# Kernel optimization log

Measured on AMD Instinct MI355X. Metric: run time of the kernel, lower is better.

The kernel has to match this reference:

```python
import jax, jax.numpy as jnp
import numpy as np

B, NELEC, NAO, NMO, NCONF, L = 128, 192, 128, 96, 32, 80
SCALE = 0.12  # keeps det of LxL matrices in float32 range


def setup_inputs() -> dict:
    key = jax.random.key(0)
    k1, k2, k3 = jax.random.split(key, 3)
    ao = jax.random.normal(k1, (B, NELEC, NAO), jnp.float32) * SCALE
    mo_w = jax.random.normal(k2, (NMO, NAO), jnp.float32) * SCALE  # Linear(nao->nmo) weight
    ci_w = jax.random.normal(k3, (1, NCONF), jnp.float32)          # Linear(nconf->1) weight
    # Configs: each config singly-occupies L distinct spatial orbitals (occ==1 branch
    # of get_index_configs -> spin-orbital index 2*i). Even, distinct, sorted indices.
    rng = np.random.default_rng(0)
    spatial = np.stack([np.sort(rng.permutation(NMO)[:L]) for _ in range(NCONF)])
    conf_idx = jnp.asarray(2 * spatial, dtype=jnp.int32)  # [NCONF, L], values < NELEC
    return {"ao": ao, "mo_w": mo_w, "ci_w": ci_w, "conf_idx": conf_idx}


def reference(ao, mo_w, ci_w, conf_idx):
    # layer_mo: mo = ao @ W^T  -> [B, NELEC, NMO]
    mo = jnp.einsum('ben,mn->bem', ao, mo_w)
    # duplicate_orbitals: stack/view/t/view == repeat each spatial orbital twice along columns
    dup = jnp.repeat(mo, 2, axis=2)  # [B, NELEC, 2*NMO]
    # SlaterPooling: gather rows and cols by the same config index, then determinant
    sub = dup[:, conf_idx[:, :, None], conf_idx[:, None, :]]  # [B, NCONF, L, L]
    dets = jnp.linalg.det(sub)  # [B, NCONF]  (batched LU)
    # layer_ci: CI-coefficient contraction -> [B, 1]
    return dets @ ci_w.T
```

## Files before the change

kernel.cpp:

```cpp
#include <hip/hip_runtime.h>

#define B_    128
#define NELEC 192
#define NAO   128
#define NMO   96
#define NCONF 32
#define L_    80

__global__ void zero_out_k(float* out) { if (threadIdx.x < B_) out[threadIdx.x] = 0.f; }

__global__ __launch_bounds__(256) void gemm_g_k(const float* __restrict__ ao,
                                                const float* __restrict__ mo_w,
                                                float* __restrict__ G) {
    int b  = blockIdx.x;
    int st = blockIdx.y;
    int tid = threadIdx.x;
    int s_local = tid >> 4;
    int m0 = (tid & 15) * 6;
    int s = st * 16 + s_local;
    const float* arow = ao + ((size_t)b * NELEC + 2 * s) * NAO;
    const float* w0   = mo_w + (size_t)m0 * NAO;
    float acc[6] = {0.f, 0.f, 0.f, 0.f, 0.f, 0.f};
    for (int n = 0; n < NAO; n += 4) {
        float4 av = *(const float4*)(arow + n);
#pragma unroll
        for (int q = 0; q < 6; ++q) {
            float4 wv = *(const float4*)(w0 + (size_t)q * NAO + n);
            acc[q] += av.x * wv.x + av.y * wv.y + av.z * wv.z + av.w * wv.w;
        }
    }
    float* grow = G + ((size_t)b * NMO + s) * NMO + m0;
#pragma unroll
    for (int q = 0; q < 6; ++q) grow[q] = acc[q];
}

__device__ __forceinline__ float rdlane(float x, int src) {
    return __int_as_float(__builtin_amdgcn_readlane(__float_as_int(x), src));
}
__device__ __forceinline__ int rdlanei(int x, int src) {
    return __builtin_amdgcn_readlane(x, src);
}
#define DPPMAX(v, ctrl)                                                          \
    v = fmaxf(v, __int_as_float(__builtin_amdgcn_update_dpp(                     \
            __float_as_int(v), __float_as_int(v), (ctrl), 0xf, 0xf, false)))

template <bool USE_G>
__global__ __launch_bounds__(64) void det_reg_k(const float* __restrict__ ao,
                                                const float* __restrict__ mo_w,
                                                const float* __restrict__ G,
                                                const float* __restrict__ ci_w,
                                                const int* __restrict__ conf_idx,
                                                float* __restrict__ out) {
    __shared__ __align__(16) float Ms[40][84];
    __shared__ int sIdx[L_];
    __shared__ int tbl[64];

    int c = blockIdx.x;
    int b = blockIdx.y;
    int lane = threadIdx.x;

    if (lane < 64) sIdx[lane] = conf_idx[c * L_ + lane] >> 1;
    if (lane < 16) sIdx[64 + lane] = conf_idx[c * L_ + 64 + lane] >> 1;
    __syncthreads();

    float a[81];
#pragma unroll
    for (int t = 0; t < 81; ++t) a[t] = 0.f;

    const float* Gb = G + (size_t)b * NMO * NMO;

#pragma unroll 1
    for (int pass = 0; pass < 2; ++pass) {
        int r0 = pass * 40;
        for (int e = lane; e < 40 * L_; e += 64) {
            int i = e / L_, j = e - i * L_;
            float v;
            if (USE_G) {
                v = Gb[(size_t)sIdx[r0 + i] * NMO + sIdx[j]];
            } else {
                const float* ar = ao + ((size_t)b * NELEC + 2 * sIdx[r0 + i]) * NAO;
                const float* wr = mo_w + (size_t)sIdx[j] * NAO;
                float acc = 0.f;
                for (int n = 0; n < NAO; n += 4) {
                    float4 av = *(const float4*)(ar + n);
                    float4 wv = *(const float4*)(wr + n);
                    acc += av.x * wv.x + av.y * wv.y + av.z * wv.z + av.w * wv.w;
                }
                v = acc;
            }
            Ms[i][j] = v;
        }
        __syncthreads();
        if (pass == 0) {
            if (lane < 40) {
#pragma unroll
                for (int q = 0; q < 20; ++q) {
                    float4 v4 = *(const float4*)&Ms[lane][4 * q];
                    a[4 * q] = v4.x; a[4 * q + 1] = v4.y; a[4 * q + 2] = v4.z; a[4 * q + 3] = v4.w;
                }
            }
        } else {
            if (lane >= 40) {
#pragma unroll
                for (int q = 0; q < 20; ++q) {
                    float4 v4 = *(const float4*)&Ms[lane - 40][4 * q];
                    a[4 * q] = v4.x; a[4 * q + 1] = v4.y; a[4 * q + 2] = v4.z; a[4 * q + 3] = v4.w;
                }
            }
        }
        __syncthreads();
    }

    double det = 1.0;
    int inv = 0;
    bool act = true;

#pragma unroll 1
    for (int k = 0; k < 16; ++k) {
        int rem = 79 - k;
        float cand = act ? fabsf(a[0]) : -1.f;
        float m = cand;
        DPPMAX(m, 0x111); DPPMAX(m, 0x112); DPPMAX(m, 0x114); DPPMAX(m, 0x118);
        DPPMAX(m, 0x142); DPPMAX(m, 0x143);
        float mx = rdlane(m, 63);
        unsigned long long sel = __ballot(act && cand == mx);
        int p = __ffsll(sel) - 1;

        inv += __popcll(__ballot(act && lane < p));

        float piv = rdlane(a[0], p);
        det *= (double)piv;
        if (lane == p) act = false;
        float la = (act && piv != 0.f) ? a[0] / piv : 0.f;

        if (lane < 16) {
            float* Brow = &Ms[24 + lane][0];
            float4 Qc = *(const float4*)&Brow[0];
            float lb = (piv != 0.f) ? Qc.x / piv : 0.f;
#pragma unroll
            for (int tb = 0; tb < 5; ++tb) {
                if (16 * tb < rem) {
#pragma unroll
                    for (int j = 0; j < 4; ++j) {
                        float4 Qn = *(const float4*)&Brow[16 * tb + 4 * j + 4];
                        float4 W;
                        W.x = fmaf(-lb, rdlane(a[16 * tb + 4 * j + 1], p), Qc.y);
                        W.y = fmaf(-lb, rdlane(a[16 * tb + 4 * j + 2], p), Qc.z);
                        W.z = fmaf(-lb, rdlane(a[16 * tb + 4 * j + 3], p), Qc.w);
                        W.w = fmaf(-lb, rdlane(a[16 * tb + 4 * j + 4], p), Qn.x);
                        *(float4*)&Brow[16 * tb + 4 * j] = W;
                        Qc = Qn;
                    }
                }
            }
        }

#pragma unroll
        for (int tb = 0; tb < 5; ++tb) {
            if (16 * tb < rem) {
#pragma unroll
                for (int i = 0; i < 16; ++i) {
                    float u = rdlane(a[16 * tb + i + 1], p);
                    a[16 * tb + i] = fmaf(-la, u, a[16 * tb + i + 1]);
                }
            }
        }
    }

    unsigned long long mask_a = __ballot(act);
    int rank = __popcll(mask_a & ((1ull << lane) - 1));
    if (act) tbl[rank] = lane;
    __syncthreads();
    int srcl = tbl[lane & 63];
    int src2 = (lane < 48) ? srcl : lane;
#pragma unroll
    for (int t = 0; t < 64; ++t) a[t] = __shfl(a[t], src2);
    if (lane >= 48) {
        const float* Brow = &Ms[24 + (lane - 48)][0];
#pragma unroll
        for (int q = 0; q < 16; ++q) {
            float4 v4 = *(const float4*)&Brow[4 * q];
            a[4 * q] = v4.x; a[4 * q + 1] = v4.y; a[4 * q + 2] = v4.z; a[4 * q + 3] = v4.w;
        }
    }
    int rowid = (lane < 48) ? srcl : (16 + lane);
    act = true;

#pragma unroll 1
    for (int k = 16; k < 80; ++k) {
        int rem = 79 - k;
        float cand = act ? fabsf(a[0]) : -1.f;
        float m = cand;
        DPPMAX(m, 0x111); DPPMAX(m, 0x112); DPPMAX(m, 0x114); DPPMAX(m, 0x118);
        DPPMAX(m, 0x142); DPPMAX(m, 0x143);
        float mx = rdlane(m, 63);
        unsigned long long sel = __ballot(act && cand == mx);
        int p = __ffsll(sel) - 1;

        int pr = rdlanei(rowid, p);
        inv += __popcll(__ballot(act && rowid < pr));

        float piv = rdlane(a[0], p);
        det *= (double)piv;
        if (lane == p) act = false;
        float la = (act && piv != 0.f) ? a[0] / piv : 0.f;

#pragma unroll
        for (int tb = 0; tb < 4; ++tb) {
            if (16 * tb < rem) {
#pragma unroll
                for (int i = 0; i < 16; ++i) {
                    float u = rdlane(a[16 * tb + i + 1], p);
                    a[16 * tb + i] = fmaf(-la, u, a[16 * tb + i + 1]);
                }
            }
        }
    }

    if (lane == 0) {
        double sgn = (inv & 1) ? -1.0 : 1.0;
        atomicAdd(&out[b], (float)(det * sgn * (double)ci_w[c]));
    }
}

extern "C" void kernel_launch(void* const* d_in, const int* in_sizes, int n_in,
                              void* d_out, int out_size, void* d_ws, size_t ws_size,
                              hipStream_t stream) {
    const float* ao    = (const float*)d_in[0];
    const float* mo_w  = (const float*)d_in[1];
    const float* ci_w  = (const float*)d_in[2];
    const int*   conf  = (const int*)d_in[3];
    float* out = (float*)d_out;
    float* G   = (float*)d_ws;

    zero_out_k<<<dim3(1), dim3(B_), 0, stream>>>(out);

    const size_t g_need = (size_t)B_ * NMO * NMO * sizeof(float);
    if (ws_size >= g_need) {
        gemm_g_k<<<dim3(B_, 6), dim3(256), 0, stream>>>(ao, mo_w, G);
        det_reg_k<true><<<dim3(NCONF, B_), dim3(64), 0, stream>>>(ao, mo_w, G, ci_w, conf, out);
    } else {
        det_reg_k<false><<<dim3(NCONF, B_), dim3(64), 0, stream>>>(ao, mo_w, nullptr, ci_w, conf, out);
    }
}
```

Measured before the change: 321.4 us.

## Keep 64 columns in registers and spill the trailing 16 to LDS

```diff
diff --git a/kernel.cpp b/kernel.cpp
--- a/kernel.cpp
+++ b/kernel.cpp
@@ -11,10 +11,12 @@
 
 __global__ __launch_bounds__(256) void gemm_g_k(const float* __restrict__ ao,
                                                 const float* __restrict__ mo_w,
-                                                float* __restrict__ G) {
+                                                float* __restrict__ G,
+                                                float* __restrict__ out) {
     int b  = blockIdx.x;
     int st = blockIdx.y;
     int tid = threadIdx.x;
+    if (st == 0 && tid == 0) out[b] = 0.f;
     int s_local = tid >> 4;
     int m0 = (tid & 15) * 6;
     int s = st * 16 + s_local;
@@ -43,6 +45,9 @@
 #define DPPMAX(v, ctrl)                                                          \
     v = fmaxf(v, __int_as_float(__builtin_amdgcn_update_dpp(                     \
             __float_as_int(v), __float_as_int(v), (ctrl), 0xf, 0xf, false)))
+
+#define USRC(X) (((X) < 64) ? rdlane(a[((X) < 64) ? (X) : 0], p)                 \
+                            : T[p * 17 + (((X) >= 64) ? ((X) - 64) : 0)])
 
 template <bool USE_G>
 __global__ __launch_bounds__(64) void det_reg_k(const float* __restrict__ ao,
@@ -54,6 +59,7 @@
     __shared__ __align__(16) float Ms[40][84];
     __shared__ int sIdx[L_];
     __shared__ int tbl[64];
+    float* T = &Ms[0][0];
 
     int c = blockIdx.x;
     int b = blockIdx.y;
@@ -63,16 +69,15 @@
     if (lane < 16) sIdx[64 + lane] = conf_idx[c * L_ + 64 + lane] >> 1;
     __syncthreads();
 
-    float a[81];
-#pragma unroll
-    for (int t = 0; t < 81; ++t) a[t] = 0.f;
-
+    float a[64];
+    float4 tl0, tl1, tl2, tl3;
     const float* Gb = G + (size_t)b * NMO * NMO;
 
 #pragma unroll 1
-    for (int pass = 0; pass < 2; ++pass) {
-        int r0 = pass * 40;
-        for (int e = lane; e < 40 * L_; e += 64) {
+    for (int pass = 0; pass < 3; ++pass) {
+        int r0 = pass * 27;
+        int nrows = (pass == 2) ? 26 : 27;
+        for (int e = lane; e < nrows * L_; e += 64) {
             int i = e / L_, j = e - i * L_;
             float v;
             if (USE_G) {
@@ -88,25 +93,27 @@
                 }
                 v = acc;
             }
-            Ms[i][j] = v;
+            Ms[13 + i][j] = v;
         }
         __syncthreads();
-        if (pass == 0) {
-            if (lane < 40) {
-#pragma unroll
-                for (int q = 0; q < 20; ++q) {
-                    float4 v4 = *(const float4*)&Ms[lane][4 * q];
-                    a[4 * q] = v4.x; a[4 * q + 1] = v4.y; a[4 * q + 2] = v4.z; a[4 * q + 3] = v4.w;
-                }
-            }
-        } else {
-            if (lane >= 40) {
-#pragma unroll
-                for (int q = 0; q < 20; ++q) {
-                    float4 v4 = *(const float4*)&Ms[lane - 40][4 * q];
-                    a[4 * q] = v4.x; a[4 * q + 1] = v4.y; a[4 * q + 2] = v4.z; a[4 * q + 3] = v4.w;
-                }
-            }
+        bool mine = (lane >= r0) && (lane < r0 + nrows) && (lane < 64);
+        if (mine) {
+            const float* R = &Ms[13 + (lane - r0)][0];
+#pragma unroll
+            for (int q = 0; q < 16; ++q) {
+                float4 v4 = *(const float4*)&R[4 * q];
+                a[4 * q] = v4.x; a[4 * q + 1] = v4.y; a[4 * q + 2] = v4.z; a[4 * q + 3] = v4.w;
+            }
+            tl0 = *(const float4*)&R[64]; tl1 = *(const float4*)&R[68];
+            tl2 = *(const float4*)&R[72]; tl3 = *(const float4*)&R[76];
+        }
+        __syncthreads();
+        if (mine) {
+            float* Tr = &T[lane * 17];
+            Tr[0]  = tl0.x; Tr[1]  = tl0.y; Tr[2]  = tl0.z; Tr[3]  = tl0.w;
+            Tr[4]  = tl1.x; Tr[5]  = tl1.y; Tr[6]  = tl1.z; Tr[7]  = tl1.w;
+            Tr[8]  = tl2.x; Tr[9]  = tl2.y; Tr[10] = tl2.z; Tr[11] = tl2.w;
+            Tr[12] = tl3.x; Tr[13] = tl3.y; Tr[14] = tl3.z; Tr[15] = tl3.w;
         }
         __syncthreads();
     }
@@ -117,7 +124,6 @@
 
 #pragma unroll 1
     for (int k = 0; k < 16; ++k) {
-        int rem = 79 - k;
         float cand = act ? fabsf(a[0]) : -1.f;
         float m = cand;
         DPPMAX(m, 0x111); DPPMAX(m, 0x112); DPPMAX(m, 0x114); DPPMAX(m, 0x118);
@@ -125,16 +131,16 @@
         float mx = rdlane(m, 63);
         unsigned long long sel = __ballot(act && cand == mx);
         int p = __ffsll(sel) - 1;
-
         inv += __popcll(__ballot(act && lane < p));
-
         float piv = rdlane(a[0], p);
         det *= (double)piv;
         if (lane == p) act = false;
         float la = (act && piv != 0.f) ? a[0] / piv : 0.f;
+        int w = 16 - k;
+        int rem = 79 - k;
 
         if (lane < 16) {
-            float* Brow = &Ms[24 + lane][0];
+            float* Brow = &Ms[23 + lane][0];
             float4 Qc = *(const float4*)&Brow[0];
             float lb = (piv != 0.f) ? Qc.x / piv : 0.f;
 #pragma unroll
@@ -144,10 +150,10 @@
                     for (int j = 0; j < 4; ++j) {
                         float4 Qn = *(const float4*)&Brow[16 * tb + 4 * j + 4];
                         float4 W;
-                        W.x = fmaf(-lb, rdlane(a[16 * tb + 4 * j + 1], p), Qc.y);
-                        W.y = fmaf(-lb, rdlane(a[16 * tb + 4 * j + 2], p), Qc.z);
-                        W.z = fmaf(-lb, rdlane(a[16 * tb + 4 * j + 3], p), Qc.w);
-                        W.w = fmaf(-lb, rdlane(a[16 * tb + 4 * j + 4], p), Qn.x);
+                        W.x = fmaf(-lb, USRC(16 * tb + 4 * j + 1), Qc.y);
+                        W.y = fmaf(-lb, USRC(16 * tb + 4 * j + 2), Qc.z);
+                        W.z = fmaf(-lb, USRC(16 * tb + 4 * j + 3), Qc.w);
+                        W.w = fmaf(-lb, USRC(16 * tb + 4 * j + 4), Qn.x);
                         *(float4*)&Brow[16 * tb + 4 * j] = W;
                         Qc = Qn;
                     }
@@ -155,13 +161,29 @@
             }
         }
 
-#pragma unroll
-        for (int tb = 0; tb < 5; ++tb) {
-            if (16 * tb < rem) {
-#pragma unroll
-                for (int i = 0; i < 16; ++i) {
-                    float u = rdlane(a[16 * tb + i + 1], p);
-                    a[16 * tb + i] = fmaf(-la, u, a[16 * tb + i + 1]);
+        float myT0 = T[lane * 17];
+        float uT0  = T[p * 17];
+#pragma unroll
+        for (int tb = 0; tb < 4; ++tb) {
+#pragma unroll
+            for (int i = 0; i < 16; ++i) {
+                int t = 16 * tb + i;
+                if (t < 63) {
+                    float u = rdlane(a[t + 1], p);
+                    a[t] = fmaf(-la, u, a[t + 1]);
+                }
+            }
+        }
+        a[63] = fmaf(-la, uT0, myT0);
+
+        if (act) {
+            float* Tr = &T[lane * 17];
+#pragma unroll
+            for (int j = 0; j < 15; ++j) {
+                if (j < w - 1) {
+                    float tn = Tr[j + 1];
+                    float un = T[p * 17 + j + 1];
+                    Tr[j] = fmaf(-la, un, tn);
                 }
             }
         }
@@ -176,7 +198,7 @@
 #pragma unroll
     for (int t = 0; t < 64; ++t) a[t] = __shfl(a[t], src2);
     if (lane >= 48) {
-        const float* Brow = &Ms[24 + (lane - 48)][0];
+        const float* Brow = &Ms[23 + (lane - 48)][0];
 #pragma unroll
         for (int q = 0; q < 16; ++q) {
             float4 v4 = *(const float4*)&Brow[4 * q];
@@ -210,8 +232,11 @@
             if (16 * tb < rem) {
 #pragma unroll
                 for (int i = 0; i < 16; ++i) {
-                    float u = rdlane(a[16 * tb + i + 1], p);
-                    a[16 * tb + i] = fmaf(-la, u, a[16 * tb + i + 1]);
+                    int t = 16 * tb + i;
+                    if (t < 63) {
+                        float u = rdlane(a[t + 1], p);
+                        a[t] = fmaf(-la, u, a[t + 1]);
+                    }
                 }
             }
         }
@@ -233,13 +258,12 @@
     float* out = (float*)d_out;
     float* G   = (float*)d_ws;
 
-    zero_out_k<<<dim3(1), dim3(B_), 0, stream>>>(out);
-
     const size_t g_need = (size_t)B_ * NMO * NMO * sizeof(float);
     if (ws_size >= g_need) {
-        gemm_g_k<<<dim3(B_, 6), dim3(256), 0, stream>>>(ao, mo_w, G);
+        gemm_g_k<<<dim3(B_, 6), dim3(256), 0, stream>>>(ao, mo_w, G, out);
         det_reg_k<true><<<dim3(NCONF, B_), dim3(64), 0, stream>>>(ao, mo_w, G, ci_w, conf, out);
     } else {
+        zero_out_k<<<dim3(1), dim3(B_), 0, stream>>>(out);
         det_reg_k<false><<<dim3(NCONF, B_), dim3(64), 0, stream>>>(ao, mo_w, nullptr, ci_w, conf, out);
     }
 }
```

After: 356.5 us. 1.11x slower.
